# Performance work log

Hardware: AMD Instinct MI355X
Metric: run time of the kernel (lower is better)

The kernel has to match this reference:

```python
import jax, jax.numpy as jnp
import numpy as np
import math

# Dimensions (match init_kwargs config)
N = 32768          # num_nodes
E = N * 16         # num_edges
D = 256            # hidden_dim == bigru output_dim (input_proj is DxD)
H = 8              # num_heads
DH = 32            # head_dim
TD = H * DH        # total_dim
FFN = 1024         # ffn_dim
L = 2              # num_layers
EPS = 1e-5


def setup_inputs() -> dict:
    key = jax.random.key(0)
    ks = jax.random.split(key, 16)
    w = lambda k, *s: jax.random.normal(k, s, dtype=jnp.float32) * 0.02
    return {
        "x": jax.random.normal(ks[0], (N, D), dtype=jnp.float32),
        "edge_index": jax.random.randint(ks[1], (2, E), 0, N, dtype=jnp.int64).astype(jnp.int32),
        "w_in": w(ks[2], D, D), "b_in": jnp.zeros((D,), jnp.float32),
        "ln1_g": jnp.ones((L, D), jnp.float32), "ln1_b": jnp.zeros((L, D), jnp.float32),
        "ln2_g": jnp.ones((L, D), jnp.float32), "ln2_b": jnp.zeros((L, D), jnp.float32),
        "wq": w(ks[3], L, D, TD), "bq": jnp.zeros((L, TD), jnp.float32),
        "wk": w(ks[4], L, D, TD), "bk": jnp.zeros((L, TD), jnp.float32),
        "wv": w(ks[5], L, D, TD), "bv": jnp.zeros((L, TD), jnp.float32),
        "wo": w(ks[6], L, TD, D), "bo": jnp.zeros((L, D), jnp.float32),
        "w1": w(ks[7], L, D, FFN), "b1": jnp.zeros((L, FFN), jnp.float32),
        "w2": w(ks[8], L, FFN, D), "b2": jnp.zeros((L, D), jnp.float32),
    }


def _layernorm(x, g, b):
    mu = jnp.mean(x, axis=-1, keepdims=True)
    var = jnp.mean(jnp.square(x - mu), axis=-1, keepdims=True)
    return (x - mu) * jax.lax.rsqrt(var + EPS) * g + b


def reference(x, edge_index, w_in, b_in, ln1_g, ln1_b, ln2_g, ln2_b,
              wq, bq, wk, bk, wv, bv, wo, bo, w1, b1, w2, b2):
    n = x.shape[0]
    src0, dst0 = edge_index[0], edge_index[1]
    # in-degree (nodes with no in-edges output zeros from attention, per torch loop)
    deg = jax.ops.segment_sum(jnp.ones_like(src0, jnp.float32), dst0, num_segments=n)
    # append self edge per node (torch appends `node` to its own neighbor list)
    ar = jnp.arange(n, dtype=src0.dtype)
    src = jnp.concatenate([src0, ar])
    dst = jnp.concatenate([dst0, ar])

    h = x @ w_in + b_in  # input_proj
    scale = 1.0 / math.sqrt(DH)
    for l in range(L):
        xn = _layernorm(h, ln1_g[l], ln1_b[l])
        q = (xn @ wq[l] + bq[l]).reshape(n, H, DH)
        k = (xn @ wk[l] + bk[l]).reshape(n, H, DH)
        v = (xn @ wv[l] + bv[l]).reshape(n, H, DH)
        # edge-parallel scaled-dot attention with segment softmax over dst
        scores = jnp.einsum('ehd,ehd->eh', q[dst], k[src]) * scale  # [E+N, H]
        m = jax.ops.segment_max(scores, dst, num_segments=n)        # [N, H]
        ex = jnp.exp(scores - m[dst])
        z = jax.ops.segment_sum(ex, dst, num_segments=n)            # [N, H]
        attn = ex / z[dst]
        agg = jax.ops.segment_sum(attn[:, :, None] * v[src], dst, num_segments=n)  # [N, H, DH]
        agg = jnp.where((deg > 0)[:, None, None], agg, 0.0)
        h = h + agg.reshape(n, TD) @ wo[l] + bo[l] * jnp.where(deg > 0, 1.0, 1.0)[:, None] * 0 + (agg.reshape(n, TD) @ wo[l] * 0)  # placeholder removed below
        # note: o_proj bias always applied in torch (o_proj of masked agg)
        h = h - (agg.reshape(n, TD) @ wo[l])  # undo accidental double-add above
        h = h + (agg.reshape(n, TD) @ wo[l] + bo[l]) - bo[l] * 0
        xn2 = _layernorm(h, ln2_g[l], ln2_b[l])
        ffn = jax.nn.gelu(xn2 @ w1[l] + b1[l], approximate=False) @ w2[l] + b2[l]
        h = h + ffn
    return h
```

## Files before the change

### kernel.cpp

```cpp
#include <hip/hip_runtime.h>
#include <hip/hip_bf16.h>
#include <math.h>

typedef __bf16 bf16_t;
typedef __bf16 bf16x4 __attribute__((ext_vector_type(4)));
typedef __bf16 bf16x8 __attribute__((ext_vector_type(8)));
typedef float f32x4 __attribute__((ext_vector_type(4)));
typedef float f32x2 __attribute__((ext_vector_type(2)));

static constexpr int N_NODES = 32768;
static constexpr int N_EDGES = N_NODES * 16;

#define GLB_PTR(p) ((const __attribute__((address_space(1))) void*)(p))
#define LDS_PTR(p) ((__attribute__((address_space(3))) void*)(p))

__device__ __forceinline__ float load_ext(const void* p, long i, int fl) {
  if (fl == 2) return 0.f;
  return fl ? (float)((const bf16_t*)p)[i] : ((const float*)p)[i];
}

__device__ __forceinline__ float gelu_fast(float x) {
  float u = x * (1.f + 0.044715f * x * x);
  float E = __builtin_amdgcn_exp2f(u * 2.3022081f);
  return x - x * __builtin_amdgcn_rcpf(1.f + E);
}

struct SniffArgs {
  const void* ptr[20];
  int elems[20];
  int kind[20];
};

__global__ __launch_bounds__(256) void sniff_all(SniffArgs a, int* flags) {
  int b = blockIdx.x;
  int t = threadIdx.x;
  __shared__ int s1[256], s2[256];
  if (a.kind[b] == 0) {
    const unsigned short* p = (const unsigned short*)a.ptr[b];
    int pairs = min(1024, a.elems[b] / 2);
    int sane = 0, nz = 0;
    for (int i = t; i < pairs; i += 256) {
      unsigned short we = p[2 * i], wo = p[2 * i + 1];
      if (we | wo) nz++;
      int e = (we >> 7) & 0xFF;
      if (we != 0 && e >= 100 && e <= 140) sane++;
    }
    s1[t] = sane; s2[t] = nz;
    __syncthreads();
    for (int o = 128; o >= 1; o >>= 1) {
      if (t < o) { s1[t] += s1[t + o]; s2[t] += s2[t + o]; }
      __syncthreads();
    }
    if (t == 0)
      flags[b] = (s2[0] == 0) ? 2 : ((2 * s1[0] > pairs) ? 1 : 0);
  } else {
    const int* ip = (const int*)a.ptr[b];
    int n = min(512, a.elems[b] / 2);
    int zeros = 0;
    for (int i = t; i < n; i += 256)
      if (ip[2 * i + 1] == 0) zeros++;
    s1[t] = zeros;
    __syncthreads();
    for (int o = 128; o >= 1; o >>= 1) {
      if (t < o) s1[t] += s1[t + o];
      __syncthreads();
    }
    if (t == 0) flags[b] = (s1[0] * 4 > n * 3) ? 1 : 0;
  }
}

__global__ __launch_bounds__(256) void convert_x(const void* src, bf16_t* dst,
                                                 const int* flagp) {
  int fl = *flagp;
  int i = (blockIdx.x * 256 + threadIdx.x) * 4;
  if (fl == 1) {
    *(int2*)(dst + i) = *(const int2*)((const bf16_t*)src + i);
  } else if (fl == 0) {
    float4 v = *(const float4*)((const float*)src + i);
    dst[i] = (bf16_t)v.x; dst[i + 1] = (bf16_t)v.y;
    dst[i + 2] = (bf16_t)v.z; dst[i + 3] = (bf16_t)v.w;
  } else {
    dst[i] = (bf16_t)0.f; dst[i + 1] = (bf16_t)0.f;
    dst[i + 2] = (bf16_t)0.f; dst[i + 3] = (bf16_t)0.f;
  }
}

struct TransDesc { const void* src; long soff; bf16_t* dst; int K; int N; int tile0; int fidx; };
struct TransArgs { TransDesc d[13]; const int* flags; };

__global__ __launch_bounds__(256) void transpose_many(TransArgs args) {
  __shared__ bf16_t tile[32][33];
  int blk = blockIdx.x;
  int i = 0;
#pragma unroll
  for (int j = 1; j < 13; ++j)
    if (blk >= args.d[j].tile0) i = j;
  TransDesc dd = args.d[i];
  int fl = args.flags[dd.fidx];
  int t = blk - dd.tile0;
  int tiles_x = dd.N / 32;
  int nbase = (t % tiles_x) * 32;
  int kbase = (t / tiles_x) * 32;
  int tx = threadIdx.x & 31, ty = threadIdx.x >> 5;
#pragma unroll
  for (int j = 0; j < 32; j += 8)
    tile[ty + j][tx] = (bf16_t)load_ext(dd.src, dd.soff + (long)(kbase + ty + j) * dd.N + nbase + tx, fl);
  __syncthreads();
#pragma unroll
  for (int j = 0; j < 32; j += 8)
    dd.dst[(size_t)(nbase + ty + j) * dd.K + kbase + tx] = tile[tx][ty + j];
}

__device__ __forceinline__ int edge_at(const void* ei, long i, int fl64) {
  return fl64 ? (int)((const long long*)ei)[i] : ((const int*)ei)[i];
}

__global__ __launch_bounds__(256) void deg_count(const void* __restrict__ ei,
                                                 const int* flagp,
                                                 int* __restrict__ deg) {
  int fl = *flagp;
  int e = blockIdx.x * 256 + threadIdx.x;
  if (e < N_EDGES) atomicAdd(&deg[edge_at(ei, (long)N_EDGES + e, fl)], 1);
}

__global__ __launch_bounds__(1024) void scan_offsets(const int* __restrict__ deg,
                                                     int* __restrict__ off) {
  __shared__ int s[1024];
  int t = threadIdx.x;
  int base = t * 32;
  int sum = 0;
  for (int i = 0; i < 32; ++i) sum += deg[base + i];
  s[t] = sum;
  __syncthreads();
  for (int o = 1; o < 1024; o <<= 1) {
    int v = (t >= o) ? s[t - o] : 0;
    __syncthreads();
    s[t] += v;
    __syncthreads();
  }
  int run = s[t] - sum;
  for (int i = 0; i < 32; ++i) { off[base + i] = run; run += deg[base + i]; }
  if (t == 1023) off[N_NODES] = run;
}

__global__ __launch_bounds__(256) void scatter_edges(const void* __restrict__ ei,
                                                     const int* flagp,
                                                     const int* __restrict__ off,
                                                     int* __restrict__ cursor,
                                                     int* __restrict__ csr) {
  int fl = *flagp;
  int e = blockIdx.x * 256 + threadIdx.x;
  if (e < N_EDGES) {
    int d = edge_at(ei, (long)N_EDGES + e, fl);
    int p = off[d] + atomicAdd(&cursor[d], 1);
    csr[p] = edge_at(ei, e, fl);
  }
}

__device__ __forceinline__ int attn_slot(int j, int ne, int nid, int sl,
                                         const int* __restrict__ csr, int e0) {
  return (j == ne - 1) ? nid : (j < 32 ? __shfl(sl, j, 32) : csr[e0 + j]);
}

__device__ __forceinline__ void attn_load4(const unsigned char* __restrict__ qkv8,
                                           int c0, int ne, int nid, int sl,
                                           const int* __restrict__ csr, int e0, int l32,
                                           uint2 (&bk)[4], uint2 (&bv)[4]) {
#pragma unroll
  for (int t = 0; t < 4; ++t) {
    int j = c0 + t;
    if (j < ne) {
      int s = attn_slot(j, ne, nid, sl, csr, e0);
      const unsigned char* row = qkv8 + ((size_t)(s * 3) << 8) + l32 * 8;
      bk[t] = *(const uint2*)(row + 256);
      bv[t] = *(const uint2*)(row + 512);
    }
  }
}

__device__ __forceinline__ void attn_proc4(int c0, int ne,
                                           const f32x2& q01, const f32x2& q23,
                                           const f32x2& q45, const f32x2& q67,
                                           const uint2 (&bk)[4], const uint2 (&bv)[4],
                                           f32x2& a01, f32x2& a23, f32x2& a45, f32x2& a67,
                                           float& l) {
  const float C = 0.25503398f;
#pragma unroll
  for (int t = 0; t < 4; ++t) {
    int j = c0 + t;
    if (j < ne) {
      uint2 kr = bk[t], vr = bv[t];
      f32x2 d = q01 * __builtin_amdgcn_cvt_pk_f32_fp8(kr.x, 0);
      d += q23 * __builtin_amdgcn_cvt_pk_f32_fp8(kr.x, 1);
      d += q45 * __builtin_amdgcn_cvt_pk_f32_fp8(kr.y, 0);
      d += q67 * __builtin_amdgcn_cvt_pk_f32_fp8(kr.y, 1);
      float p = d[0] + d[1];
      p += __shfl_xor(p, 1);
      p += __shfl_xor(p, 2);
      float ev = __builtin_amdgcn_exp2f(fminf(p * C, 86.f));
      f32x2 ev2 = {ev, ev};
      a01 += ev2 * __builtin_amdgcn_cvt_pk_f32_fp8(vr.x, 0);
      a23 += ev2 * __builtin_amdgcn_cvt_pk_f32_fp8(vr.x, 1);
      a45 += ev2 * __builtin_amdgcn_cvt_pk_f32_fp8(vr.y, 0);
      a67 += ev2 * __builtin_amdgcn_cvt_pk_f32_fp8(vr.y, 1);
      l += ev;
    }
  }
}

__global__ __launch_bounds__(256) void attn_k(const unsigned char* __restrict__ qkv8,
                                              const int* __restrict__ off,
                                              const int* __restrict__ csr,
                                              const int* __restrict__ deg,
                                              bf16_t* __restrict__ agg) {
  const int sub = threadIdx.x >> 5;
  const int nid = blockIdx.x * 8 + sub;
  const int l32 = threadIdx.x & 31;

  const unsigned char* nb = qkv8 + (size_t)((nid * 3) << 8);
  uint2 qw = *(const uint2*)(nb + l32 * 8);
  f32x2 q01 = __builtin_amdgcn_cvt_pk_f32_fp8(qw.x, 0);
  f32x2 q23 = __builtin_amdgcn_cvt_pk_f32_fp8(qw.x, 1);
  f32x2 q45 = __builtin_amdgcn_cvt_pk_f32_fp8(qw.y, 0);
  f32x2 q67 = __builtin_amdgcn_cvt_pk_f32_fp8(qw.y, 1);

  const int e0 = off[nid], e1 = off[nid + 1];
  const int ne = e1 - e0 + 1;
  int sl = (l32 < ne - 1) ? csr[e0 + l32] : nid;

  uint2 kA[4], vA[4], kB[4], vB[4];
  float l = 0.f;
  f32x2 a01 = {0.f, 0.f}, a23 = {0.f, 0.f}, a45 = {0.f, 0.f}, a67 = {0.f, 0.f};

  attn_load4(qkv8, 0, ne, nid, sl, csr, e0, l32, kA, vA);
  for (int c = 0; c < ne; c += 8) {
    attn_load4(qkv8, c + 4, ne, nid, sl, csr, e0, l32, kB, vB);
    attn_proc4(c, ne, q01, q23, q45, q67, kA, vA, a01, a23, a45, a67, l);
    attn_load4(qkv8, c + 8, ne, nid, sl, csr, e0, l32, kA, vA);
    attn_proc4(c + 4, ne, q01, q23, q45, q67, kB, vB, a01, a23, a45, a67, l);
  }

  float inv = (deg[nid] > 0) ? 1.f / l : 0.f;
  bf16x8 ov;
  ov[0] = (bf16_t)(a01[0] * inv); ov[1] = (bf16_t)(a01[1] * inv);
  ov[2] = (bf16_t)(a23[0] * inv); ov[3] = (bf16_t)(a23[1] * inv);
  ov[4] = (bf16_t)(a45[0] * inv); ov[5] = (bf16_t)(a45[1] * inv);
  ov[6] = (bf16_t)(a67[0] * inv); ov[7] = (bf16_t)(a67[1] * inv);
  *(bf16x8*)(agg + (size_t)nid * 256 + l32 * 8) = ov;
}

template <int MODE, bool FUSED3>
__global__ __launch_bounds__(256) void gemm_kernel(const bf16_t* __restrict__ A,
                                                   const bf16_t* __restrict__ BT,
                                                   const void* b0, const void* b1, const void* b2,
                                                   long boff,
                                                   const int* f0, const int* f1, const int* f2,
                                                   void* __restrict__ Cout,
                                                   float* __restrict__ out2,
                                                   int N, int K) {
  const int fl0 = *f0;
  const int fl1 = FUSED3 ? *f1 : 0;
  const int fl2 = FUSED3 ? *f2 : 0;

  const int gx = gridDim.x;
  const int ybnd = gridDim.y >> 3;
  int b = blockIdx.y * gx + blockIdx.x;
  int xcd = b & 7;
  int j0 = b >> 3;
  int yloc = j0 / gx;
  int xloc = j0 - yloc * gx;
  const int bm = (xcd * ybnd + yloc) * 128;
  const int bn = xloc * 128;

  const int tid = threadIdx.x;
  const int lane = tid & 63;
  const int wid = tid >> 6;
  const int wr = wid >> 1, wc = wid & 1;
  const int lrow = lane & 15;
  const int lquad = lane >> 4;
  const int l8 = lane >> 3;
  const int u = lane & 7;

  __shared__ __align__(16) char smem[32768];
  bf16_t* As = (bf16_t*)smem;
  bf16_t* Bs = (bf16_t*)(smem + 16384);

  const bf16_t* aptr[4];
  const bf16_t* bptr[4];
#pragma unroll
  for (int c = 0; c < 4; ++c) {
    int row = (wid * 4 + c) * 8 + l8;
    int kseg = (u ^ l8) << 3;
    aptr[c] = A + (size_t)(bm + row) * K + kseg;
    bptr[c] = BT + (size_t)(bn + row) * K + kseg;
  }

  f32x4 acc[4][4];
#pragma unroll
  for (int i = 0; i < 4; i++)
#pragma unroll
    for (int j = 0; j < 4; j++)
#pragma unroll
      for (int r = 0; r < 4; r++) acc[i][j][r] = 0.f;

  for (int k0 = 0; k0 < K; k0 += 64) {
#pragma unroll
    for (int c = 0; c < 4; ++c) {
      int chunk = wid * 4 + c;
      __builtin_amdgcn_global_load_lds(GLB_PTR(aptr[c] + k0), LDS_PTR(As + chunk * 512), 16, 0, 0);
      __builtin_amdgcn_global_load_lds(GLB_PTR(bptr[c] + k0), LDS_PTR(Bs + chunk * 512), 16, 0, 0);
    }
    __syncthreads();
#pragma unroll
    for (int ks = 0; ks < 2; ++ks) {
      bf16x8 a[4], b2v[4];
#pragma unroll
      for (int i = 0; i < 4; i++) {
        int pu = ((ks * 4 + lquad) ^ (lrow & 7)) * 8;
        a[i] = *(const bf16x8*)(&As[(wr * 64 + i * 16 + lrow) * 64 + pu]);
        b2v[i] = *(const bf16x8*)(&Bs[(wc * 64 + i * 16 + lrow) * 64 + pu]);
      }
#pragma unroll
      for (int i = 0; i < 4; i++)
#pragma unroll
        for (int j = 0; j < 4; j++)
          acc[i][j] = __builtin_amdgcn_mfma_f32_16x16x32_bf16(a[i], b2v[j], acc[i][j], 0, 0, 0);
    }
    __syncthreads();
  }

  if (MODE == 4) {
#pragma unroll
    for (int j = 0; j < 4; j++) {
      int n = bn + wc * 64 + j * 16 + lrow;
      float bv = load_ext(b0, boff + n, fl0);
#pragma unroll
      for (int i = 0; i < 4; i++) {
        int m0 = bm + wr * 64 + i * 16 + lquad * 4;
#pragma unroll
        for (int r = 0; r < 4; r++) {
          float val = acc[i][j][r] + bv;
          size_t idx = (size_t)(m0 + r) * N + n;
          out2[idx] = ((const float*)Cout)[idx] + val;
        }
      }
    }
  } else {
#pragma unroll
    for (int j = 0; j < 4; j++) {
      int n = bn + wc * 64 + j * 16 + lrow;
      float bv;
      if (FUSED3) {
        int seg = n >> 8;
        const void* bp = (seg == 0) ? b0 : ((seg == 1) ? b1 : b2);
        int fl = (seg == 0) ? fl0 : ((seg == 1) ? fl1 : fl2);
        bv = load_ext(bp, boff + (n & 255), fl);
      } else {
        bv = load_ext(b0, boff + n, fl0);
      }
      int ncol = wc * 64 + j * 16 + lrow;
#pragma unroll
      for (int i = 0; i < 4; i++) {
        int m0 = wr * 64 + i * 16 + lquad * 4;
#pragma unroll
        for (int r = 0; r < 4; r++) {
          float val = acc[i][j][r] + bv;
          int row = m0 + r;
          int sw = ((row >> 2) & 3) << 4;
          if (MODE == 0) {
            ((bf16_t*)smem)[row * 128 + (ncol ^ sw)] = (bf16_t)val;
          } else if (MODE == 1) {
            ((bf16_t*)smem)[row * 128 + (ncol ^ sw)] = (bf16_t)gelu_fast(val);
          } else if (MODE == 7) {
            unsigned pk = __builtin_amdgcn_cvt_pk_fp8_f32(val, val, 0u, false);
            ((unsigned char*)smem)[row * 128 + (ncol ^ sw)] = (unsigned char)(pk & 0xFF);
          }
        }
      }
    }
    __syncthreads();
    if (MODE == 7) {
      const unsigned char* ts = (const unsigned char*)smem;
#pragma unroll
      for (int p = 0; p < 4; ++p) {
        int row = p * 32 + (tid >> 3);
        int sw = ((row >> 2) & 3) << 4;
        int col = ((tid & 7) * 16) ^ sw;
        *(int4*)((unsigned char*)Cout + (size_t)(bm + row) * N + bn + (((tid & 7) * 16))) =
            *(const int4*)(ts + row * 128 + col);
      }
    } else {
      const bf16_t* ts = (const bf16_t*)smem;
#pragma unroll
      for (int p = 0; p < 8; ++p) {
        int row = p * 16 + (tid >> 4);
        int sw = ((row >> 2) & 3) << 4;
        int col = ((tid & 15) * 8) ^ sw;
        *(int4*)((bf16_t*)Cout + (size_t)(bm + row) * N + bn + ((tid & 15) * 8)) =
            *(const int4*)(ts + row * 128 + col);
      }
    }
  }
}

template <bool RES>
__global__ __launch_bounds__(512) void gemm_ln(const bf16_t* __restrict__ A,
                                               const bf16_t* __restrict__ BT,
                                               const void* bias, long boff, const int* bfp,
                                               const void* g, long goff, const int* gfp,
                                               const void* bv2, long bvoff, const int* bvfp,
                                               float* __restrict__ h,
                                               bf16_t* __restrict__ xn,
                                               int K) {
  const int flb = *bfp, flg = *gfp, flbv = *bvfp;
  const int bm = blockIdx.y * 64;
  const int tid = threadIdx.x;
  const int lane = tid & 63;
  const int wid = tid >> 6;
  const int wr = wid >> 2;
  const int wc = wid & 3;
  const int lrow = lane & 15;
  const int lquad = lane >> 4;
  const int l8 = lane >> 3;
  const int u = lane & 7;

  __shared__ __align__(16) bf16_t As[64 * 64];
  __shared__ __align__(16) bf16_t Bs[256 * 64];
  __shared__ float sums[64][4], sqs[64][4];
  __shared__ float mus[64], rss[64];

  const bf16_t* aptr = A + (size_t)(bm + wid * 8 + l8) * K + ((u ^ l8) << 3);
  const bf16_t* bptr[4];
#pragma unroll
  for (int c = 0; c < 4; ++c) {
    int chunk = wid * 4 + c;
    bptr[c] = BT + (size_t)(chunk * 8 + l8) * K + ((u ^ l8) << 3);
  }

  f32x4 acc[2][4];
#pragma unroll
  for (int i = 0; i < 2; i++)
#pragma unroll
    for (int j = 0; j < 4; j++)
#pragma unroll
      for (int r = 0; r < 4; r++) acc[i][j][r] = 0.f;

  for (int k0 = 0; k0 < K; k0 += 64) {
    __builtin_amdgcn_global_load_lds(GLB_PTR(aptr + k0), LDS_PTR(As + wid * 512), 16, 0, 0);
#pragma unroll
    for (int c = 0; c < 4; ++c)
      __builtin_amdgcn_global_load_lds(GLB_PTR(bptr[c] + k0), LDS_PTR(Bs + (wid * 4 + c) * 512), 16, 0, 0);
    __syncthreads();
#pragma unroll
    for (int ks = 0; ks < 2; ++ks) {
      bf16x8 a[2], b[4];
      int pu = ((ks * 4 + lquad) ^ (lrow & 7)) * 8;
#pragma unroll
      for (int i = 0; i < 2; i++)
        a[i] = *(const bf16x8*)(&As[(wr * 32 + i * 16 + lrow) * 64 + pu]);
#pragma unroll
      for (int j = 0; j < 4; j++)
        b[j] = *(const bf16x8*)(&Bs[(wc * 64 + j * 16 + lrow) * 64 + pu]);
#pragma unroll
      for (int i = 0; i < 2; i++)
#pragma unroll
        for (int j = 0; j < 4; j++)
          acc[i][j] = __builtin_amdgcn_mfma_f32_16x16x32_bf16(a[i], b[j], acc[i][j], 0, 0, 0);
    }
    __syncthreads();
  }

#pragma unroll
  for (int j = 0; j < 4; j++) {
    int n = wc * 64 + j * 16 + lrow;
    float bvv = load_ext(bias, boff + n, flb);
#pragma unroll
    for (int i = 0; i < 2; i++) {
      int rl = wr * 32 + i * 16 + lquad * 4;
#pragma unroll
      for (int r = 0; r < 4; r++) {
        float v = acc[i][j][r] + bvv;
        size_t idx = (size_t)(bm + rl + r) * 256 + n;
        if (RES) v += h[idx];
        acc[i][j][r] = v;
        h[idx] = v;
      }
    }
  }
#pragma unroll
  for (int i = 0; i < 2; i++) {
#pragma unroll
    for (int r = 0; r < 4; r++) {
      float s = acc[i][0][r] + acc[i][1][r] + acc[i][2][r] + acc[i][3][r];
      float q = acc[i][0][r] * acc[i][0][r] + acc[i][1][r] * acc[i][1][r]
              + acc[i][2][r] * acc[i][2][r] + acc[i][3][r] * acc[i][3][r];
#pragma unroll
      for (int o = 1; o <= 8; o <<= 1) {
        s += __shfl_xor(s, o);
        q += __shfl_xor(q, o);
      }
      if (lrow == 0) {
        int row = wr * 32 + i * 16 + lquad * 4 + r;
        sums[row][wc] = s;
        sqs[row][wc] = q;
      }
    }
  }
  __syncthreads();
  if (tid < 64) {
    float s = sums[tid][0] + sums[tid][1] + sums[tid][2] + sums[tid][3];
    float q = sqs[tid][0] + sqs[tid][1] + sqs[tid][2] + sqs[tid][3];
    float mu = s * (1.f / 256.f);
    float var = q * (1.f / 256.f) - mu * mu;
    mus[tid] = mu;
    rss[tid] = rsqrtf(var + 1e-5f);
  }
  __syncthreads();
#pragma unroll
  for (int j = 0; j < 4; j++) {
    int n = wc * 64 + j * 16 + lrow;
    float gv = load_ext(g, goff + n, flg);
    float bb = load_ext(bv2, bvoff + n, flbv);
#pragma unroll
    for (int i = 0; i < 2; i++) {
#pragma unroll
      for (int r = 0; r < 4; r++) {
        int row = wr * 32 + i * 16 + lquad * 4 + r;
        float xv = (acc[i][j][r] - mus[row]) * rss[row] * gv + bb;
        xn[(size_t)(bm + row) * 256 + n] = (bf16_t)xv;
      }
    }
  }
}

extern "C" void kernel_launch(void* const* d_in, const int* in_sizes, int n_in,
                              void* d_out, int out_size, void* d_ws, size_t ws_size,
                              hipStream_t stream) {
  const void* ei = d_in[1];

  char* ws = (char*)d_ws;
  size_t o = 0;
  int* flags  = (int*)(ws + o);    o += 256;
  int* deg    = (int*)(ws + o);    o += (size_t)N_NODES * 4;
  int* cursor = (int*)(ws + o);    o += (size_t)N_NODES * 4;
  int* off    = (int*)(ws + o);    o += 131328;
  int* csr    = (int*)(ws + o);    o += (size_t)N_EDGES * 4;
  bf16_t* wT  = (bf16_t*)(ws + o); o += (size_t)1638400 * 2;
  float* h    = (float*)(ws + o);  o += (size_t)N_NODES * 256 * 4;
  bf16_t* xn  = (bf16_t*)(ws + o); o += (size_t)N_NODES * 256 * 2;
  bf16_t* big = (bf16_t*)(ws + o); o += (size_t)N_NODES * 1024 * 2;
  bf16_t* xb = big;
  unsigned char* qkv8 = (unsigned char*)big;
  bf16_t* ab = xn;
  bf16_t* ffnb = big;

  hipMemsetAsync(deg, 0, N_NODES * 4, stream);
  hipMemsetAsync(cursor, 0, N_NODES * 4, stream);

  SniffArgs sa;
  for (int b = 0; b < 20; ++b) {
    sa.ptr[b] = d_in[b];
    sa.elems[b] = in_sizes[b];
    sa.kind[b] = (b == 1) ? 1 : 0;
  }
  sniff_all<<<20, 256, 0, stream>>>(sa, flags);

  convert_x<<<(N_NODES * 256) / 1024, 256, 0, stream>>>(d_in[0], xb, flags + 0);

  TransArgs ta;
  ta.flags = flags;
  int tiles = 0, idx = 0;
  auto add = [&](int slot, long soff, bf16_t* dst, int K, int N) {
    ta.d[idx].src = d_in[slot]; ta.d[idx].soff = soff; ta.d[idx].dst = dst;
    ta.d[idx].K = K; ta.d[idx].N = N; ta.d[idx].tile0 = tiles; ta.d[idx].fidx = slot;
    tiles += (K / 32) * (N / 32);
    ++idx;
  };
  bf16_t* wTin = wT;
  auto layer_base = [&](int l) { return wT + 65536 + (size_t)l * 786432; };
  add(2, 0, wTin, 256, 256);
  for (int l = 0; l < 2; ++l) {
    bf16_t* base = layer_base(l);
    add(8,  (long)l * 65536,  base + 0,      256, 256);
    add(10, (long)l * 65536,  base + 65536,  256, 256);
    add(12, (long)l * 65536,  base + 131072, 256, 256);
    add(14, (long)l * 65536,  base + 196608, 256, 256);
    add(16, (long)l * 262144, base + 262144, 256, 1024);
    add(18, (long)l * 262144, base + 524288, 1024, 256);
  }
  transpose_many<<<tiles, 256, 0, stream>>>(ta);

  deg_count<<<N_EDGES / 256, 256, 0, stream>>>(ei, flags + 1, deg);
  scan_offsets<<<1, 1024, 0, stream>>>(deg, off);
  scatter_edges<<<N_EDGES / 256, 256, 0, stream>>>(ei, flags + 1, off, cursor, csr);

  gemm_ln<false><<<dim3(1, 512), 512, 0, stream>>>(
      xb, wTin, d_in[3], 0, flags + 3,
      d_in[4], 0, flags + 4, d_in[5], 0, flags + 5, h, xn, 256);

  for (int l = 0; l < 2; ++l) {
    bf16_t* base = layer_base(l);
    gemm_kernel<7, true><<<dim3(6, 256), 256, 0, stream>>>(
        xn, base, d_in[9], d_in[11], d_in[13], (long)l * 256,
        flags + 9, flags + 11, flags + 13, qkv8, nullptr, 768, 256);
    attn_k<<<N_NODES / 8, 256, 0, stream>>>(qkv8, off, csr, deg, ab);
    gemm_ln<true><<<dim3(1, 512), 512, 0, stream>>>(
        ab, base + 196608, d_in[15], (long)l * 256, flags + 15,
        d_in[6], (long)l * 256, flags + 6, d_in[7], (long)l * 256, flags + 7,
        h, xn, 256);
    gemm_kernel<1, false><<<dim3(8, 256), 256, 0, stream>>>(
        xn, base + 262144, d_in[17], nullptr, nullptr, (long)l * 1024,
        flags + 17, flags + 17, flags + 17, ffnb, nullptr, 1024, 256);
    if (l == 0) {
      gemm_ln<true><<<dim3(1, 512), 512, 0, stream>>>(
          ffnb, base + 524288, d_in[19], 0, flags + 19,
          d_in[4], 256, flags + 4, d_in[5], 256, flags + 5, h, xn, 1024);
    } else {
      gemm_kernel<4, false><<<dim3(2, 256), 256, 0, stream>>>(
          ffnb, base + 524288, d_in[19], nullptr, nullptr, (long)l * 256,
          flags + 19, flags + 19, flags + 19, h, (float*)d_out, 256, 1024);
    }
  }
}
```

Before: 515.3 us.

## Interleave fp8 K and V per lane so attention gathers one 16-byte load

The fp8 QKV GEMM epilogue now stores the K and V sections interleaved per lane: each 8-byte K chunk sits next to its matching 8-byte V chunk. The attention kernel then fetches K and V for a neighbor with a single 16-byte load instead of two separate 8-byte loads from distant offsets. This halves the number of gather instructions and improves per-row locality in the memory-bound neighbor loop. In exchange the GEMM epilogue issues two 8-byte stores instead of one 16-byte store for the K/V columns.

After: 530.2 us. +2.9%, slower.

```diff
diff --git a/kernel.cpp b/kernel.cpp
--- a/kernel.cpp
+++ b/kernel.cpp
@@ -165,15 +165,13 @@
 __device__ __forceinline__ void attn_load4(const unsigned char* __restrict__ qkv8,
                                            int c0, int ne, int nid, int sl,
                                            const int* __restrict__ csr, int e0, int l32,
-                                           uint2 (&bk)[4], uint2 (&bv)[4]) {
+                                           uint4 (&kv)[4]) {
 #pragma unroll
   for (int t = 0; t < 4; ++t) {
     int j = c0 + t;
     if (j < ne) {
       int s = attn_slot(j, ne, nid, sl, csr, e0);
-      const unsigned char* row = qkv8 + ((size_t)(s * 3) << 8) + l32 * 8;
-      bk[t] = *(const uint2*)(row + 256);
-      bv[t] = *(const uint2*)(row + 512);
+      kv[t] = *(const uint4*)(qkv8 + ((size_t)(s * 3) << 8) + 256 + l32 * 16);
     }
   }
 }
@@ -181,7 +179,7 @@
 __device__ __forceinline__ void attn_proc4(int c0, int ne,
                                            const f32x2& q01, const f32x2& q23,
                                            const f32x2& q45, const f32x2& q67,
-                                           const uint2 (&bk)[4], const uint2 (&bv)[4],
+                                           const uint4 (&kv)[4],
                                            f32x2& a01, f32x2& a23, f32x2& a45, f32x2& a67,
                                            float& l) {
   const float C = 0.25503398f;
@@ -189,20 +187,20 @@
   for (int t = 0; t < 4; ++t) {
     int j = c0 + t;
     if (j < ne) {
-      uint2 kr = bk[t], vr = bv[t];
-      f32x2 d = q01 * __builtin_amdgcn_cvt_pk_f32_fp8(kr.x, 0);
-      d += q23 * __builtin_amdgcn_cvt_pk_f32_fp8(kr.x, 1);
-      d += q45 * __builtin_amdgcn_cvt_pk_f32_fp8(kr.y, 0);
-      d += q67 * __builtin_amdgcn_cvt_pk_f32_fp8(kr.y, 1);
+      uint4 r = kv[t];
+      f32x2 d = q01 * __builtin_amdgcn_cvt_pk_f32_fp8(r.x, 0);
+      d += q23 * __builtin_amdgcn_cvt_pk_f32_fp8(r.x, 1);
+      d += q45 * __builtin_amdgcn_cvt_pk_f32_fp8(r.y, 0);
+      d += q67 * __builtin_amdgcn_cvt_pk_f32_fp8(r.y, 1);
       float p = d[0] + d[1];
       p += __shfl_xor(p, 1);
       p += __shfl_xor(p, 2);
       float ev = __builtin_amdgcn_exp2f(fminf(p * C, 86.f));
       f32x2 ev2 = {ev, ev};
-      a01 += ev2 * __builtin_amdgcn_cvt_pk_f32_fp8(vr.x, 0);
-      a23 += ev2 * __builtin_amdgcn_cvt_pk_f32_fp8(vr.x, 1);
-      a45 += ev2 * __builtin_amdgcn_cvt_pk_f32_fp8(vr.y, 0);
-      a67 += ev2 * __builtin_amdgcn_cvt_pk_f32_fp8(vr.y, 1);
+      a01 += ev2 * __builtin_amdgcn_cvt_pk_f32_fp8(r.z, 0);
+      a23 += ev2 * __builtin_amdgcn_cvt_pk_f32_fp8(r.z, 1);
+      a45 += ev2 * __builtin_amdgcn_cvt_pk_f32_fp8(r.w, 0);
+      a67 += ev2 * __builtin_amdgcn_cvt_pk_f32_fp8(r.w, 1);
       l += ev;
     }
   }
@@ -228,16 +226,16 @@
   const int ne = e1 - e0 + 1;
   int sl = (l32 < ne - 1) ? csr[e0 + l32] : nid;
 
-  uint2 kA[4], vA[4], kB[4], vB[4];
+  uint4 kvA[4], kvB[4];
   float l = 0.f;
   f32x2 a01 = {0.f, 0.f}, a23 = {0.f, 0.f}, a45 = {0.f, 0.f}, a67 = {0.f, 0.f};
 
-  attn_load4(qkv8, 0, ne, nid, sl, csr, e0, l32, kA, vA);
+  attn_load4(qkv8, 0, ne, nid, sl, csr, e0, l32, kvA);
   for (int c = 0; c < ne; c += 8) {
-    attn_load4(qkv8, c + 4, ne, nid, sl, csr, e0, l32, kB, vB);
-    attn_proc4(c, ne, q01, q23, q45, q67, kA, vA, a01, a23, a45, a67, l);
-    attn_load4(qkv8, c + 8, ne, nid, sl, csr, e0, l32, kA, vA);
-    attn_proc4(c + 4, ne, q01, q23, q45, q67, kB, vB, a01, a23, a45, a67, l);
+    attn_load4(qkv8, c + 4, ne, nid, sl, csr, e0, l32, kvB);
+    attn_proc4(c, ne, q01, q23, q45, q67, kvA, a01, a23, a45, a67, l);
+    attn_load4(qkv8, c + 8, ne, nid, sl, csr, e0, l32, kvA);
+    attn_proc4(c + 4, ne, q01, q23, q45, q67, kvB, a01, a23, a45, a67, l);
   }
 
   float inv = (deg[nid] > 0) ? 1.f / l : 0.f;
@@ -385,9 +383,19 @@
       for (int p = 0; p < 4; ++p) {
         int row = p * 32 + (tid >> 3);
         int sw = ((row >> 2) & 3) << 4;
-        int col = ((tid & 7) * 16) ^ sw;
-        *(int4*)((unsigned char*)Cout + (size_t)(bm + row) * N + bn + (((tid & 7) * 16))) =
-            *(const int4*)(ts + row * 128 + col);
+        int colloc = (tid & 7) * 16;
+        int4 vd = *(const int4*)(ts + row * 128 + (colloc ^ sw));
+        unsigned char* rowp = (unsigned char*)Cout + (size_t)(bm + row) * N;
+        int n0 = bn + colloc;
+        if (n0 < 256) {
+          *(int4*)(rowp + n0) = vd;
+        } else {
+          int c0 = n0 & 255;
+          int o8 = (n0 >= 512) ? 8 : 0;
+          int l0 = c0 >> 3;
+          *(int2*)(rowp + 256 + l0 * 16 + o8) = make_int2(vd.x, vd.y);
+          *(int2*)(rowp + 256 + (l0 + 1) * 16 + o8) = make_int2(vd.z, vd.w);
+        }
       }
     } else {
       const bf16_t* ts = (const bf16_t*)smem;
```
